# Kernel tuning notes

Measured on AMD Instinct MI355X. Metric: run time of the kernel, lower is better.

The kernel has to match this reference:

```python
import jax, jax.numpy as jnp
import numpy as np

B, N, K, D = 8, 4096, 26, 64


def setup_inputs() -> dict:
    key = jax.random.key(0)
    ks = jax.random.split(key, 7)
    return {
        "targets": jax.random.normal(ks[0], (B, N, D), dtype=jnp.float32),
        "neighbors": jax.random.normal(ks[1], (B, N, K, D), dtype=jnp.float32),
        "a": jax.random.uniform(ks[2], (B, N, K), dtype=jnp.float32),
        "kernel_target": jax.random.normal(ks[3], (1, 1, D), dtype=jnp.float32) * 0.1,
        "bias_target": jax.random.normal(ks[4], (1, 1, D), dtype=jnp.float32) * 0.1,
        "kernel_neighbor": jax.random.normal(ks[5], (1, 1, D), dtype=jnp.float32) * 0.1,
        "bias_neighbor": jax.random.normal(ks[6], (1, 1, 1, D), dtype=jnp.float32) * 0.1,
    }


def reference(targets, neighbors, a, kernel_target, bias_target, kernel_neighbor, bias_neighbor):
    # Faithful to the TF call(), including the broadcast quirk:
    # targets (B,N,D) * kernel_neighbor (1,1,D) + bias_neighbor (1,1,1,D) -> (1,B,N,D)
    t = targets * kernel_neighbor + bias_neighbor            # (1,B,N,D)
    n = neighbors * kernel_target + bias_target              # (B,N,K,D)
    # expand_dims(t, -2) -> (1,B,N,1,D); product with n and a[...,None] -> (1,B,N,K,D);
    # reduce_sum over axis=2 (the N axis of the rank-5 tensor) -> (1,B,K,D).
    # Expressed as a fused einsum to avoid materializing the rank-5 intermediate.
    w = jnp.einsum("zbnd,bnkd,bnk->zbkd", t, n, a)           # (1,B,K,D)
    return jax.nn.sigmoid(w)
```

## Files before the change

### kernel.cpp

```cpp
#include <hip/hip_runtime.h>
#include <math.h>

#define BB 8
#define NN 4096
#define KK 26
#define DD 64
#define CH 64
#define NPB (NN / CH)

__global__ __launch_bounds__(256) void gat_partial(
    const float* __restrict__ targets,
    const float* __restrict__ neighbors,
    const float* __restrict__ a,
    const float* __restrict__ kt,
    const float* __restrict__ bt,
    const float* __restrict__ kn,
    const float* __restrict__ bn,
    float* __restrict__ out)
{
    const int b     = blockIdx.x / CH;
    const int chunk = blockIdx.x % CH;
    const int tid   = threadIdx.x;
    const int wave  = tid >> 6;
    const int lane  = tid & 63;
    const int d     = lane;

    const float kt_d = kt[d];
    const float bt_d = bt[d];
    const float kn_d = kn[d];
    const float bn_d = bn[d];

    float acc[KK];
#pragma unroll
    for (int k = 0; k < KK; ++k) acc[k] = 0.f;

    const int n0 = chunk * NPB;
    for (int n = n0 + wave; n < n0 + NPB; n += 4) {
        const size_t row = (size_t)(b * NN + n);
        const float tt = fmaf(targets[row * DD + d], kn_d, bn_d);
        const float* __restrict__ nbrow = neighbors + row * (size_t)(KK * DD);
        const float* __restrict__ arow  = a + row * KK;
#pragma unroll
        for (int k = 0; k < KK; ++k) {
            const float av = arow[k];
            const float nb = nbrow[k * DD + d];
            acc[k] = fmaf(tt * av, fmaf(nb, kt_d, bt_d), acc[k]);
        }
    }

    __shared__ float lds[4][KK * DD];
#pragma unroll
    for (int k = 0; k < KK; ++k) lds[wave][k * DD + lane] = acc[k];
    __syncthreads();

    for (int idx = tid; idx < KK * DD; idx += 256) {
        const float s = lds[0][idx] + lds[1][idx] + lds[2][idx] + lds[3][idx];
        atomicAdd(&out[b * (KK * DD) + idx], s);
    }
}

__global__ __launch_bounds__(256) void gat_sigmoid(float* __restrict__ out, int nelem) {
    const int i = blockIdx.x * blockDim.x + threadIdx.x;
    if (i < nelem) {
        const float x = out[i];
        out[i] = 1.f / (1.f + expf(-x));
    }
}

extern "C" void kernel_launch(void* const* d_in, const int* in_sizes, int n_in,
                              void* d_out, int out_size, void* d_ws, size_t ws_size,
                              hipStream_t stream) {
    const float* targets = (const float*)d_in[0];
    const float* neighbors = (const float*)d_in[1];
    const float* a = (const float*)d_in[2];
    const float* kt = (const float*)d_in[3];
    const float* bt = (const float*)d_in[4];
    const float* kn = (const float*)d_in[5];
    const float* bn = (const float*)d_in[6];
    float* out = (float*)d_out;

    hipMemsetAsync(d_out, 0, (size_t)out_size * sizeof(float), stream);

    gat_partial<<<BB * CH, 256, 0, stream>>>(targets, neighbors, a, kt, bt, kn, bn, out);
    gat_sigmoid<<<(out_size + 255) / 256, 256, 0, stream>>>(out, out_size);
}
```

Baseline: 46.93 us.

## Replace atomics with workspace reduction, vectorize loads, fuse sigmoid into reduce

Each block now writes its partial K×D sums to a workspace slot instead of issuing atomicAdds. A second kernel sums the chunks and applies the sigmoid, which removes the memset and the separate sigmoid pass. Neighbor rows are read with float4/float2 vector loads, and the chunk count is doubled for more blocks. The path depends on workspace size and falls back to the atomic version, at the cost of extra workspace traffic.

```diff
diff --git a/kernel.cpp b/kernel.cpp
--- a/kernel.cpp
+++ b/kernel.cpp
@@ -5,17 +5,124 @@
 #define NN 4096
 #define KK 26
 #define DD 64
-#define CH 64
+#define CH 128
 #define NPB (NN / CH)
+#define KD (KK * DD)
 
-__global__ __launch_bounds__(256) void gat_partial(
+__global__ __launch_bounds__(256) void gat_partial_ws(
     const float* __restrict__ targets,
     const float* __restrict__ neighbors,
     const float* __restrict__ a,
-    const float* __restrict__ kt,
-    const float* __restrict__ bt,
-    const float* __restrict__ kn,
-    const float* __restrict__ bn,
+    const float* __restrict__ kt, const float* __restrict__ bt,
+    const float* __restrict__ kn, const float* __restrict__ bn,
+    float* __restrict__ ws)
+{
+    const int b     = blockIdx.x / CH;
+    const int chunk = blockIdx.x % CH;
+    const int tid   = threadIdx.x;
+    const int wave  = tid >> 6;
+    const int lane  = tid & 63;
+
+    const int g16 = lane >> 4, r16 = lane & 15;
+    const int g32 = lane >> 5, r32 = lane & 31;
+
+    const float4 kt4 = ((const float4*)kt)[r16];
+    const float4 bt4 = ((const float4*)bt)[r16];
+    const float4 kn4 = ((const float4*)kn)[r16];
+    const float4 bn4 = ((const float4*)bn)[r16];
+    const float2 kt2 = ((const float2*)kt)[r32];
+    const float2 bt2 = ((const float2*)bt)[r32];
+    const float2 kn2 = ((const float2*)kn)[r32];
+    const float2 bn2 = ((const float2*)bn)[r32];
+
+    float4 acc4[6];
+#pragma unroll
+    for (int kk = 0; kk < 6; ++kk) acc4[kk] = make_float4(0.f, 0.f, 0.f, 0.f);
+    float2 accT = make_float2(0.f, 0.f);
+
+    const int n0 = chunk * NPB;
+    for (int n = n0 + wave; n < n0 + NPB; n += 4) {
+        const size_t row = (size_t)(b * NN + n);
+        const float4 t4 = ((const float4*)(targets + row * DD))[r16];
+        const float2 t2 = ((const float2*)(targets + row * DD))[r32];
+        float4 tt4;
+        tt4.x = fmaf(t4.x, kn4.x, bn4.x);
+        tt4.y = fmaf(t4.y, kn4.y, bn4.y);
+        tt4.z = fmaf(t4.z, kn4.z, bn4.z);
+        tt4.w = fmaf(t4.w, kn4.w, bn4.w);
+        float2 tt2;
+        tt2.x = fmaf(t2.x, kn2.x, bn2.x);
+        tt2.y = fmaf(t2.y, kn2.y, bn2.y);
+
+        const float4* __restrict__ nbrow4 = (const float4*)(neighbors + row * (size_t)KD);
+        const float*  __restrict__ arow   = a + row * KK;
+#pragma unroll
+        for (int kk = 0; kk < 6; ++kk) {
+            const float  av = arow[kk * 4 + g16];
+            const float4 v  = nbrow4[kk * 64 + lane];
+            acc4[kk].x = fmaf(tt4.x * av, fmaf(v.x, kt4.x, bt4.x), acc4[kk].x);
+            acc4[kk].y = fmaf(tt4.y * av, fmaf(v.y, kt4.y, bt4.y), acc4[kk].y);
+            acc4[kk].z = fmaf(tt4.z * av, fmaf(v.z, kt4.z, bt4.z), acc4[kk].z);
+            acc4[kk].w = fmaf(tt4.w * av, fmaf(v.w, kt4.w, bt4.w), acc4[kk].w);
+        }
+        {
+            const float  av = arow[24 + g32];
+            const float2 v  = ((const float2*)nbrow4)[768 + lane];
+            accT.x = fmaf(tt2.x * av, fmaf(v.x, kt2.x, bt2.x), accT.x);
+            accT.y = fmaf(tt2.y * av, fmaf(v.y, kt2.y, bt2.y), accT.y);
+        }
+    }
+
+    __shared__ float lds[4][KD];
+#pragma unroll
+    for (int kk = 0; kk < 6; ++kk)
+        ((float4*)lds[wave])[kk * 64 + lane] = acc4[kk];
+    ((float2*)lds[wave])[768 + lane] = accT;
+    __syncthreads();
+
+    float4* __restrict__ wrow4 = (float4*)(ws + ((size_t)b * CH + chunk) * KD);
+    for (int i4 = tid; i4 < KD / 4; i4 += 256) {
+        const float4 v0 = ((const float4*)lds[0])[i4];
+        const float4 v1 = ((const float4*)lds[1])[i4];
+        const float4 v2 = ((const float4*)lds[2])[i4];
+        const float4 v3 = ((const float4*)lds[3])[i4];
+        float4 s;
+        s.x = (v0.x + v1.x) + (v2.x + v3.x);
+        s.y = (v0.y + v1.y) + (v2.y + v3.y);
+        s.z = (v0.z + v1.z) + (v2.z + v3.z);
+        s.w = (v0.w + v1.w) + (v2.w + v3.w);
+        wrow4[i4] = s;
+    }
+}
+
+__global__ __launch_bounds__(256) void gat_reduce_sigmoid(
+    const float* __restrict__ ws, float* __restrict__ out)
+{
+    const int i = blockIdx.x * 256 + threadIdx.x;
+    const int total = BB * (KD / 4);
+    if (i >= total) return;
+    const int b = i / (KD / 4);
+    const int j = i % (KD / 4);
+    const float4* __restrict__ wsb = (const float4*)(ws + (size_t)b * CH * KD) + j;
+    float4 s = make_float4(0.f, 0.f, 0.f, 0.f);
+#pragma unroll 4
+    for (int c = 0; c < CH; ++c) {
+        const float4 v = wsb[(size_t)c * (KD / 4)];
+        s.x += v.x; s.y += v.y; s.z += v.z; s.w += v.w;
+    }
+    float4 o;
+    o.x = 1.f / (1.f + expf(-s.x));
+    o.y = 1.f / (1.f + expf(-s.y));
+    o.z = 1.f / (1.f + expf(-s.z));
+    o.w = 1.f / (1.f + expf(-s.w));
+    ((float4*)out)[i] = o;
+}
+
+__global__ __launch_bounds__(256) void gat_partial_atomic(
+    const float* __restrict__ targets, const float* __restrict__ neighbors,
+    const float* __restrict__ a,
+    const float* __restrict__ kt, const float* __restrict__ bt,
+    const float* __restrict__ kn, const float* __restrict__ bn,
     float* __restrict__ out)
 {
     const int b     = blockIdx.x / CH;
@@ -24,63 +131,55 @@
     const int wave  = tid >> 6;
     const int lane  = tid & 63;
     const int d     = lane;
-
-    const float kt_d = kt[d];
-    const float bt_d = bt[d];
-    const float kn_d = kn[d];
-    const float bn_d = bn[d];
-
+    const float kt_d = kt[d], bt_d = bt[d], kn_d = kn[d], bn_d = bn[d];
     float acc[KK];
 #pragma unroll
     for (int k = 0; k < KK; ++k) acc[k] = 0.f;
-
     const int n0 = chunk * NPB;
     for (int n = n0 + wave; n < n0 + NPB; n += 4) {
         const size_t row = (size_t)(b * NN + n);
         const float tt = fmaf(targets[row * DD + d], kn_d, bn_d);
-        const float* __restrict__ nbrow = neighbors + row * (size_t)(KK * DD);
+        const float* __restrict__ nbrow = neighbors + row * (size_t)KD;
         const float* __restrict__ arow  = a + row * KK;
 #pragma unroll
-        for (int k = 0; k < KK; ++k) {
-            const float av = arow[k];
-            const float nb = nbrow[k * DD + d];
-            acc[k] = fmaf(tt * av, fmaf(nb, kt_d, bt_d), acc[k]);
-        }
+        for (int k = 0; k < KK; ++k)
+            acc[k] = fmaf(tt * arow[k], fmaf(nbrow[k * DD + d], kt_d, bt_d), acc[k]);
     }
-
-    __shared__ float lds[4][KK * DD];
+    __shared__ float lds[4][KD];
 #pragma unroll
     for (int k = 0; k < KK; ++k) lds[wave][k * DD + lane] = acc[k];
     __syncthreads();
-
-    for (int idx = tid; idx < KK * DD; idx += 256) {
+    for (int idx = tid; idx < KD; idx += 256) {
         const float s = lds[0][idx] + lds[1][idx] + lds[2][idx] + lds[3][idx];
-        atomicAdd(&out[b * (KK * DD) + idx], s);
+        atomicAdd(&out[b * KD + idx], s);
     }
 }
 
 __global__ __launch_bounds__(256) void gat_sigmoid(float* __restrict__ out, int nelem) {
     const int i = blockIdx.x * blockDim.x + threadIdx.x;
-    if (i < nelem) {
-        const float x = out[i];
-        out[i] = 1.f / (1.f + expf(-x));
-    }
+    if (i < nelem) out[i] = 1.f / (1.f + expf(-out[i]));
 }
 
 extern "C" void kernel_launch(void* const* d_in, const int* in_sizes, int n_in,
                               void* d_out, int out_size, void* d_ws, size_t ws_size,
                               hipStream_t stream) {
-    const float* targets = (const float*)d_in[0];
+    const float* targets   = (const float*)d_in[0];
     const float* neighbors = (const float*)d_in[1];
-    const float* a = (const float*)d_in[2];
-    const float* kt = (const float*)d_in[3];
-    const float* bt = (const float*)d_in[4];
-    const float* kn = (const float*)d_in[5];
-    const float* bn = (const float*)d_in[6];
+    const float* a         = (const float*)d_in[2];
+    const float* kt        = (const float*)d_in[3];
+    const float* bt        = (const float*)d_in[4];
+    const float* kn        = (const float*)d_in[5];
+    const float* bn        = (const float*)d_in[6];
     float* out = (float*)d_out;
 
-    hipMemsetAsync(d_out, 0, (size_t)out_size * sizeof(float), stream);
-
-    gat_partial<<<BB * CH, 256, 0, stream>>>(targets, neighbors, a, kt, bt, kn, bn, out);
-    gat_sigmoid<<<(out_size + 255) / 256, 256, 0, stream>>>(out, out_size);
+    const size_t ws_need = (size_t)BB * CH * KD * sizeof(float);
+    if (ws_size >= ws_need) {
+        float* ws = (float*)d_ws;
+        gat_partial_ws<<<BB * CH, 256, 0, stream>>>(targets, neighbors, a, kt, bt, kn, bn, ws);
+        gat_reduce_sigmoid<<<(BB * (KD / 4) + 255) / 256, 256, 0, stream>>>(ws, out);
+    } else {
+        hipMemsetAsync(d_out, 0, (size_t)out_size * sizeof(float), stream);
+        gat_partial_atomic<<<BB * CH, 256, 0, stream>>>(targets, neighbors, a, kt, bt, kn, bn, out);
+        gat_sigmoid<<<(out_size + 255) / 256, 256, 0, stream>>>(out, out_size);
+    }
 }
```

New measurement: 51.61 us. 10.0% more time.
